# Kernel tuning notes

Measured on AMD Instinct MI355X. Metric: run time of the kernel, lower is better.

## Reference

```python
import jax, jax.numpy as jnp
import numpy as np

NUM_GROUPS = 32
EPS = 1e-5


def group_norm(x, w, b):
    # x: [B, C, H, W]
    B, C, H, W = x.shape
    g = x.reshape(B, NUM_GROUPS, C // NUM_GROUPS, H, W)
    mu = g.mean(axis=(2, 3, 4), keepdims=True)
    var = g.var(axis=(2, 3, 4), keepdims=True)
    g = (g - mu) * jax.lax.rsqrt(var + EPS)
    x = g.reshape(B, C, H, W)
    return x * w[None, :, None, None] + b[None, :, None, None]


def conv1x1(x, w, b):
    # 1x1 conv == channel matmul; x: [B, C, H, W], w: [O, C], b: [O]
    return jnp.einsum('bchw,oc->bohw', x, w) + b[None, :, None, None]


def setup_inputs() -> dict:
    key = jax.random.key(0)
    ks = jax.random.split(key, 11)
    C = 512
    B, H, W = 4, 64, 64
    s = 1.0 / np.sqrt(C)
    return {
        'x': jax.random.normal(ks[0], (B, C, H, W), jnp.float32),
        'gn_w': jax.random.uniform(ks[1], (C,), jnp.float32, 0.5, 1.5),
        'gn_b': jax.random.normal(ks[2], (C,), jnp.float32) * 0.1,
        'wq': jax.random.normal(ks[3], (C, C), jnp.float32) * s,
        'bq': jax.random.normal(ks[4], (C,), jnp.float32) * 0.01,
        'wk': jax.random.normal(ks[5], (C, C), jnp.float32) * s,
        'bk': jax.random.normal(ks[6], (C,), jnp.float32) * 0.01,
        'wv': jax.random.normal(ks[7], (C, C), jnp.float32) * s,
        'bv': jax.random.normal(ks[8], (C,), jnp.float32) * 0.01,
        'wo': jax.random.normal(ks[9], (C, C), jnp.float32) * s,
        'bo': jax.random.normal(ks[10], (C,), jnp.float32) * 0.01,
    }


def reference(x, gn_w, gn_b, wq, bq, wk, bk, wv, bv, wo, bo):
    B, C, H, W = x.shape
    h_ = group_norm(x, gn_w, gn_b)
    q = conv1x1(h_, wq, bq).reshape(B, C, H * W)   # [B, C, HW]
    k = conv1x1(h_, wk, bk).reshape(B, C, H * W)
    v = conv1x1(h_, wv, bv).reshape(B, C, H * W)
    # scores: q^T k, scaled by C^-0.5; softmax over keys
    scores = jnp.einsum('bci,bcj->bij', q, k) * (C ** -0.5)  # [B, HW, HW]
    attn = jax.nn.softmax(scores, axis=-1)
    # h_[b,c,i] = sum_j v[b,c,j] * attn[b,i,j]
    h_ = jnp.einsum('bcj,bij->bci', v, attn).reshape(B, C, H, W)
    return x + conv1x1(h_, wo, bo)
```

## Files before the change

### kernel.cpp

```cpp
#include <hip/hip_runtime.h>
#include <hip/hip_bf16.h>

typedef __attribute__((ext_vector_type(8))) __bf16 bf16x8;
typedef __attribute__((ext_vector_type(4))) float f32x4;

__device__ __forceinline__ unsigned short f2bf(float f) {
  union { float f; unsigned u; } v; v.f = f;
  unsigned r = v.u + 0x7fffu + ((v.u >> 16) & 1u);
  return (unsigned short)(r >> 16);
}

__device__ __forceinline__ void gload_lds16(const void* g, void* s) {
  __builtin_amdgcn_global_load_lds(
      (const __attribute__((address_space(1))) void*)g,
      (__attribute__((address_space(3))) void*)s, 16, 0, 0);
}

__global__ __launch_bounds__(256) void convert_w(
    const float* __restrict__ wq, const float* __restrict__ wk,
    const float* __restrict__ wv, const float* __restrict__ wo,
    unsigned short* __restrict__ dst) {
  const int m = blockIdx.x >> 10;
  const float* src = (m == 0) ? wq : (m == 1) ? wk : (m == 2) ? wv : wo;
  const int idx = ((blockIdx.x & 1023) << 8) | threadIdx.x;
  dst[m * 262144 + idx] = f2bf(src[idx]);
}

__global__ __launch_bounds__(256) void zero_k(float* __restrict__ p, int n) {
  const int i = blockIdx.x * 256 + threadIdx.x;
  if (i < n) p[i] = 0.f;
}

__global__ __launch_bounds__(256) void gn_stats(
    const float* __restrict__ x, float2* __restrict__ partials) {
  const int bg = blockIdx.x >> 2, part = blockIdx.x & 3;
  const float* xg = x + (size_t)bg * 65536 + part * 1024;
  const int t = threadIdx.x;
  float s = 0.f, ss = 0.f;
#pragma unroll
  for (int r = 0; r < 16; ++r) {
    const float4 v = *(const float4*)(xg + (size_t)r * 4096 + t * 4);
    s += v.x + v.y + v.z + v.w;
    ss += v.x * v.x + v.y * v.y + v.z * v.z + v.w * v.w;
  }
#pragma unroll
  for (int m = 32; m; m >>= 1) { s += __shfl_xor(s, m); ss += __shfl_xor(ss, m); }
  __shared__ float red[8];
  const int wave = t >> 6, lane = t & 63;
  if (lane == 0) { red[wave] = s; red[wave + 4] = ss; }
  __syncthreads();
  if (t == 0) {
    float2 p;
    p.x = red[0] + red[1] + red[2] + red[3];
    p.y = red[4] + red[5] + red[6] + red[7];
    partials[blockIdx.x] = p;
  }
}

__global__ __launch_bounds__(256) void gn_apply(
    const float* __restrict__ x, const float2* __restrict__ partials,
    const float* __restrict__ gw, const float* __restrict__ gb,
    unsigned short* __restrict__ h_t) {
  const int bg = blockIdx.x >> 3, cc = blockIdx.x & 7;
  const int b = bg >> 5, g = bg & 31;
  const int t = threadIdx.x;
  __shared__ float chs[32];
  __shared__ unsigned short tile[16][520];
  if (t < 16) {
    const float2 p0 = partials[bg * 4 + 0], p1 = partials[bg * 4 + 1];
    const float2 p2 = partials[bg * 4 + 2], p3 = partials[bg * 4 + 3];
    const float S = p0.x + p1.x + p2.x + p3.x;
    const float SS = p0.y + p1.y + p2.y + p3.y;
    const float mu = S * (1.f / 65536.f);
    const float rstd = rsqrtf(SS * (1.f / 65536.f) - mu * mu + 1e-5f);
    const float sc = gw[g * 16 + t] * rstd;
    chs[t] = sc;
    chs[16 + t] = gb[g * 16 + t] - mu * sc;
  }
  __syncthreads();
  const float* xg = x + (size_t)bg * 65536 + cc * 512;
#pragma unroll
  for (int rr = 0; rr < 8; ++rr) {
    const int r = rr * 2 + (t >> 7), i = (t & 127) * 4;
    const float4 v = *(const float4*)(xg + (size_t)r * 4096 + i);
    const float sc = chs[r], sh = chs[16 + r];
    ushort4 o;
    o.x = f2bf(v.x * sc + sh); o.y = f2bf(v.y * sc + sh);
    o.z = f2bf(v.z * sc + sh); o.w = f2bf(v.w * sc + sh);
    *(ushort4*)&tile[r][i] = o;
  }
  __syncthreads();
  unsigned short* outp = h_t + ((size_t)b * 4096 + cc * 512) * 512 + g * 16;
#pragma unroll
  for (int rep = 0; rep < 4; ++rep) {
    const int task = rep * 256 + t;
    const int nl = task >> 1, half = (task & 1) * 8;
    ushort4 o0, o1;
    o0.x = tile[half + 0][nl]; o0.y = tile[half + 1][nl];
    o0.z = tile[half + 2][nl]; o0.w = tile[half + 3][nl];
    o1.x = tile[half + 4][nl]; o1.y = tile[half + 5][nl];
    o1.z = tile[half + 6][nl]; o1.w = tile[half + 7][nl];
    *(ushort4*)(outp + (size_t)nl * 512 + half) = o0;
    *(ushort4*)(outp + (size_t)nl * 512 + half + 4) = o1;
  }
}

__global__ __launch_bounds__(256) void reduce4_k(
    const float* __restrict__ part, const float* __restrict__ l,
    unsigned short* __restrict__ dst) {
  const size_t i = ((size_t)blockIdx.x * 256 + threadIdx.x) * 4;
  f32x4 s0 = *(const f32x4*)(part + i);
  f32x4 s1 = *(const f32x4*)(part + 2097152 + i);
  f32x4 s2 = *(const f32x4*)(part + 4194304 + i);
  f32x4 s3 = *(const f32x4*)(part + 6291456 + i);
  f32x4 s = (s0 + s1) + (s2 + s3);
  const float inv = 1.f / l[i >> 9];
  ushort4 o;
  o.x = f2bf(s[0] * inv); o.y = f2bf(s[1] * inv);
  o.z = f2bf(s[2] * inv); o.w = f2bf(s[3] * inv);
  *(ushort4*)(dst + i) = o;
}

__global__ __launch_bounds__(512, 4) void gemm_s256(
    const unsigned short* __restrict__ A, const unsigned short* __restrict__ Bt,
    unsigned short* __restrict__ Out, float* __restrict__ lsum) {
  __shared__ __align__(16) char smem[73728];
  const int tid = threadIdx.x;
  const int wave = tid >> 6, lane = tid & 63;
  const int l15 = lane & 15, l4 = lane >> 4;
  const int wm = wave >> 1, wn = wave & 1;

  const int bz = blockIdx.z;
  A += (size_t)bz * 2097152;
  Bt += (size_t)bz * 2097152;
  Out += (size_t)bz * 16777216;
  lsum += (size_t)bz * 4096;

  const int id = blockIdx.y * 32 + blockIdx.x;
  const int xcd = id & 7, j = id >> 3;
  const int by = ((xcd >> 1) << 2) + (j >> 4);
  const int bx = ((xcd & 1) << 4) + (j & 15);
  const int row0 = by << 8, col0 = bx << 7;

  const int ar = tid >> 2;
  const int akc = (tid & 3) ^ ((tid >> 4) & 3);

  auto stage = [&](int kt, int bi) {
    const int kb = kt << 5;
    char* base = smem + bi * 24576;
    const unsigned short* gA = A + (size_t)(row0 + ar) * 512 + kb + akc * 8;
    const unsigned short* gB = Bt + (size_t)(col0 + ar) * 512 + kb + akc * 8;
    gload_lds16(gA, base + wave * 1024);
    gload_lds16(gA + (size_t)128 * 512, base + 8192 + wave * 1024);
    gload_lds16(gB, base + 16384 + wave * 1024);
  };

  f32x4 acc[4][4];
#pragma unroll
  for (int r = 0; r < 4; ++r)
#pragma unroll
    for (int c = 0; c < 4; ++c) acc[r][c] = (f32x4)0.f;

  const int xsw = (l4 ^ (l15 >> 2)) << 4;

  auto compute = [&](int bi) {
    const char* pa = smem + bi * 24576 + (wm * 64 + l15) * 64 + xsw;
    const char* pb = smem + bi * 24576 + 16384 + (wn * 64 + l15) * 64 + xsw;
    bf16x8 af[4], bfr[4];
#pragma unroll
    for (int r = 0; r < 4; ++r) af[r] = *(const bf16x8*)(pa + r * 1024);
#pragma unroll
    for (int c = 0; c < 4; ++c) bfr[c] = *(const bf16x8*)(pb + c * 1024);
#pragma unroll
    for (int r = 0; r < 4; ++r)
#pragma unroll
      for (int c = 0; c < 4; ++c)
        acc[r][c] = __builtin_amdgcn_mfma_f32_16x16x32_bf16(af[r], bfr[c], acc[r][c], 0, 0, 0);
  };

  stage(0, 0);
  stage(1, 1);
  int bi = 0;
  for (int kt = 0; kt < 15; ++kt) {
    asm volatile("s_waitcnt vmcnt(3)" ::: "memory");
    __builtin_amdgcn_s_barrier();
    __builtin_amdgcn_sched_barrier(0);
    if (kt + 2 < 16) stage(kt + 2, (kt + 2) % 3);
    compute(bi);
    bi = (bi == 2) ? 0 : bi + 1;
  }
  asm volatile("s_waitcnt vmcnt(0)" ::: "memory");
  __builtin_amdgcn_s_barrier();
  __builtin_amdgcn_sched_barrier(0);
  compute(bi);

  __syncthreads();
  unsigned short* tile = (unsigned short*)smem;
#pragma unroll
  for (int p = 0; p < 2; ++p) {
    if ((wm >> 1) == p) {
#pragma unroll
      for (int c = 0; c < 4; ++c) {
        const int coll = wn * 64 + c * 16 + l15;
#pragma unroll
        for (int r = 0; r < 4; ++r) {
          const int rowl = (wm & 1) * 64 + r * 16 + l4 * 4;
#pragma unroll
          for (int j = 0; j < 4; ++j)
            tile[(rowl + j) * 136 + coll] = f2bf(__expf(acc[r][c][j]));
        }
      }
    }
    __syncthreads();
#pragma unroll
    for (int it = 0; it < 4; ++it) {
      const int idx = it * 512 + tid;
      const int rw = idx >> 4, ch = (idx & 15) * 8;
      const uint4 vv = *(const uint4*)&tile[rw * 136 + ch];
      *(uint4*)(Out + (size_t)(row0 + p * 128 + rw) * 4096 + col0 + ch) = vv;
      const unsigned* uu = (const unsigned*)&vv;
      float s = 0.f;
#pragma unroll
      for (int q = 0; q < 4; ++q) {
        union { unsigned u; float f; } w;
        w.u = uu[q] << 16; s += w.f;
        w.u = uu[q] & 0xffff0000u; s += w.f;
      }
      s += __shfl_xor(s, 1); s += __shfl_xor(s, 2);
      s += __shfl_xor(s, 4); s += __shfl_xor(s, 8);
      if ((lane & 15) == 0) atomicAdd(&lsum[row0 + p * 128 + rw], s);
    }
    __syncthreads();
  }
}

__global__ __launch_bounds__(512, 2) void gemm_pv(
    const unsigned short* __restrict__ P, const unsigned short* __restrict__ Vt,
    unsigned short* __restrict__ Out, const float* __restrict__ lrow) {
  __shared__ __align__(16) char smem[147456];
  const int tid = threadIdx.x;
  const int wave = tid >> 6, lane = tid & 63;
  const int l15 = lane & 15, l4 = lane >> 4;
  const int wm = wave >> 1, wn = wave & 1;

  const int L = blockIdx.x + ((blockIdx.y + (blockIdx.z << 4)) << 2);
  const int xcd = L & 7, j = L >> 3;
  const int panel = xcd * 8 + (j >> 2);
  const int bx = j & 3, by = panel & 15, bz = panel >> 4;
  const int row0 = by << 8, col0 = bx << 7;
  P += (size_t)bz * 16777216;
  Vt += (size_t)bz * 2097152;
  Out += (size_t)bz * 2097152;
  lrow += bz * 4096;

  const int sr = tid >> 3;
  const int sc8 = (tid & 7) ^ (sr & 7);
  const unsigned short* gA = P + (size_t)(row0 + sr) * 4096 + sc8 * 8;
  const unsigned short* gB = Vt + (size_t)(col0 + sr) * 4096 + sc8 * 8;

  auto stA = [&](int kt, int bi, int p) {
    gload_lds16(gA + (size_t)(p << 6) * 4096 + (kt << 6),
                smem + bi * 49152 + p * 8192 + wave * 1024);
  };
  auto stB = [&](int kt, int bi, int p) {
    gload_lds16(gB + (size_t)(p << 6) * 4096 + (kt << 6),
                smem + bi * 49152 + 32768 + p * 8192 + wave * 1024);
  };

  f32x4 acc[4][4];
#pragma unroll
  for (int r = 0; r < 4; ++r)
#pragma unroll
    for (int c = 0; c < 4; ++c) acc[r][c] = (f32x4)0.f;

  const int sw0 = (l4 ^ (l15 & 7)) << 4;
  const int sw1 = ((4 + l4) ^ (l15 & 7)) << 4;
  const int arow = (wm * 64 + l15) << 7;
  const int brow = (wn * 64 + l15) << 7;

  bf16x8 bfr[4][2];

  stA(0, 0, 0); stA(0, 0, 1); stA(0, 0, 2); stA(0, 0, 3);
  stB(0, 0, 0); stB(0, 0, 1);
  stA(1, 1, 0); stA(1, 1, 1); stA(1, 1, 2); stA(1, 1, 3);
  stB(1, 1, 0); stB(1, 1, 1);
  asm volatile("s_waitcnt vmcnt(6)" ::: "memory");
  __builtin_amdgcn_s_barrier();
  __builtin_amdgcn_sched_barrier(0);

  int bi = 0;
#pragma unroll 1
  for (int kt = 0; kt < 64; ++kt) {
    const char* bufA = smem + bi * 49152;
    const char* bufB = bufA + 32768;
    const int pb = (bi + 2) % 3;
    const bool pre = (kt + 2 < 64);
    bf16x8 a0, a1;
    a0 = *(const bf16x8*)(bufA + arow + sw0);
    a1 = *(const bf16x8*)(bufA + arow + sw1);
#pragma unroll
    for (int c = 0; c < 4; ++c) {
      bfr[c][0] = *(const bf16x8*)(bufB + brow + c * 2048 + sw0);
      bfr[c][1] = *(const bf16x8*)(bufB + brow + c * 2048 + sw1);
    }
    if (pre) { stA(kt + 2, pb, 0); stA(kt + 2, pb, 1); }
    __builtin_amdgcn_s_barrier();
    asm volatile("s_waitcnt lgkmcnt(0)" ::: "memory");
    __builtin_amdgcn_sched_barrier(0);
    __builtin_amdgcn_s_setprio(1);
#pragma unroll
    for (int c = 0; c < 4; ++c) {
      acc[0][c] = __builtin_amdgcn_mfma_f32_16x16x32_bf16(a0, bfr[c][0], acc[0][c], 0, 0, 0);
      acc[0][c] = __builtin_amdgcn_mfma_f32_16x16x32_bf16(a1, bfr[c][1], acc[0][c], 0, 0, 0);
    }
    __builtin_amdgcn_s_setprio(0);
    __builtin_amdgcn_s_barrier();
    a0 = *(const bf16x8*)(bufA + arow + 2048 + sw0);
    a1 = *(const bf16x8*)(bufA + arow + 2048 + sw1);
    if (pre) { stA(kt + 2, pb, 2); stA(kt + 2, pb, 3); }
    __builtin_amdgcn_s_barrier();
    asm volatile("s_waitcnt lgkmcnt(0)" ::: "memory");
    __builtin_amdgcn_sched_barrier(0);
    __builtin_amdgcn_s_setprio(1);
#pragma unroll
    for (int c = 0; c < 4; ++c) {
      acc[1][c] = __builtin_amdgcn_mfma_f32_16x16x32_bf16(a0, bfr[c][0], acc[1][c], 0, 0, 0);
      acc[1][c] = __builtin_amdgcn_mfma_f32_16x16x32_bf16(a1, bfr[c][1], acc[1][c], 0, 0, 0);
    }
    __builtin_amdgcn_s_setprio(0);
    __builtin_amdgcn_s_barrier();
    a0 = *(const bf16x8*)(bufA + arow + 4096 + sw0);
    a1 = *(const bf16x8*)(bufA + arow + 4096 + sw1);
    if (pre) { stB(kt + 2, pb, 0); stB(kt + 2, pb, 1); }
    __builtin_amdgcn_s_barrier();
    asm volatile("s_waitcnt lgkmcnt(0)" ::: "memory");
    __builtin_amdgcn_sched_barrier(0);
    __builtin_amdgcn_s_setprio(1);
#pragma unroll
    for (int c = 0; c < 4; ++c) {
      acc[2][c] = __builtin_amdgcn_mfma_f32_16x16x32_bf16(a0, bfr[c][0], acc[2][c], 0, 0, 0);
      acc[2][c] = __builtin_amdgcn_mfma_f32_16x16x32_bf16(a1, bfr[c][1], acc[2][c], 0, 0, 0);
    }
    __builtin_amdgcn_s_setprio(0);
    __builtin_amdgcn_s_barrier();
    a0 = *(const bf16x8*)(bufA + arow + 6144 + sw0);
    a1 = *(const bf16x8*)(bufA + arow + 6144 + sw1);
    __builtin_amdgcn_s_barrier();
    asm volatile("s_waitcnt lgkmcnt(0)" ::: "memory");
    __builtin_amdgcn_sched_barrier(0);
    __builtin_amdgcn_s_setprio(1);
#pragma unroll
    for (int c = 0; c < 4; ++c) {
      acc[3][c] = __builtin_amdgcn_mfma_f32_16x16x32_bf16(a0, bfr[c][0], acc[3][c], 0, 0, 0);
      acc[3][c] = __builtin_amdgcn_mfma_f32_16x16x32_bf16(a1, bfr[c][1], acc[3][c], 0, 0, 0);
    }
    __builtin_amdgcn_s_setprio(0);
    if (pre) asm volatile("s_waitcnt vmcnt(6)" ::: "memory");
    else     asm volatile("s_waitcnt vmcnt(0)" ::: "memory");
    __builtin_amdgcn_s_barrier();
    __builtin_amdgcn_sched_barrier(0);
    bi = (bi == 2) ? 0 : bi + 1;
  }

  __syncthreads();
  unsigned short* tile = (unsigned short*)smem;
#pragma unroll
  for (int c = 0; c < 4; ++c) {
    const int coll = wn * 64 + c * 16 + l15;
#pragma unroll
    for (int r = 0; r < 4; ++r) {
      const int rowl = wm * 64 + r * 16 + l4 * 4;
#pragma unroll
      for (int j = 0; j < 4; ++j) {
        const float v = acc[r][c][j] * (1.0f / lrow[row0 + rowl + j]);
        tile[(rowl + j) * 136 + coll] = f2bf(v);
      }
    }
  }
  __syncthreads();
#pragma unroll
  for (int it = 0; it < 8; ++it) {
    const int idx = it * 512 + tid;
    const int rw = idx >> 4, ch = (idx & 15) * 8;
    const uint4 vv = *(const uint4*)&tile[rw * 136 + ch];
    *(uint4*)(Out + (size_t)(row0 + rw) * 512 + col0 + ch) = vv;
  }
}

template <bool OUT_BF16, int BIAS_MODE, bool RESID, bool TRANS_OUT, int SWZ,
          bool COAL>
__global__ __launch_bounds__(256) void gemm_bt(
    const unsigned short* __restrict__ A, long long sA, int lda,
    const unsigned short* __restrict__ Bt, long long sB, int ldb,
    void* __restrict__ OutV, long long sO, int ldo,
    const float* __restrict__ bias,
    const float* __restrict__ resid, long long sR,
    int K, float scale) {
  __shared__ __align__(16) char smem[49152];
  const int tid = threadIdx.x;
  const int wave = tid >> 6, lane = tid & 63;
  const int l15 = lane & 15, l4 = lane >> 4;
  const int wm = wave >> 1, wn = wave & 1;

  int bx = blockIdx.x, by = blockIdx.y, bz = blockIdx.z;
  if constexpr (SWZ == 1) {
    const int id = by * 32 + bx;
    const int xcd = id & 7, j = id >> 3;
    by = ((xcd >> 1) << 3) + (j >> 4);
    bx = ((xcd & 1) << 4) + (j & 15);
  } else if constexpr (SWZ == 2) {
    const int L = bx + ((by + (bz << 5)) << 2);
    const int xcd = L & 7, j = L >> 3;
    const int pair = xcd * 16 + (j >> 2);
    bx = j & 3;
    by = pair & 31;
    bz = pair >> 5;
  }
  const int row0 = by << 7, col0 = bx << 7;
  A += (size_t)bz * sA;
  Bt += (size_t)bz * sB;
  if (RESID) resid += (size_t)bz * sR;
  if constexpr (BIAS_MODE == 3) bias += (size_t)bz * sR;
  char* outB = (char*)OutV + (size_t)bz * sO * (OUT_BF16 ? 2 : 4);

  const int ar = tid >> 2;
  const int akc = (tid & 3) ^ ((tid >> 4) & 3);

  auto stage = [&](int kt, int bi) {
    const int kb = kt << 5;
    char* sAl = smem + bi * 16384 + wave * 1024;
    char* sBl = sAl + 8192;
    const unsigned short* gA = A + (size_t)(row0 + ar) * lda + kb + akc * 8;
    const unsigned short* gB = Bt + (size_t)(col0 + ar) * ldb + kb + akc * 8;
    gload_lds16(gA, sAl);
    gload_lds16(gB, sBl);
    gload_lds16(gA + (size_t)64 * lda, sAl + 4096);
    gload_lds16(gB + (size_t)64 * ldb, sBl + 4096);
  };

  f32x4 acc[4][4];
#pragma unroll
  for (int r = 0; r < 4; ++r)
#pragma unroll
    for (int c = 0; c < 4; ++c) acc[r][c] = (f32x4)0.f;

  const int nk = K >> 5;
  const int xsw = (l4 ^ (l15 >> 2)) << 4;

  auto compute = [&](int bi) {
    const char* pa = smem + bi * 16384 + (wm * 64 + l15) * 64 + xsw;
    const char* pb = smem + bi * 16384 + 8192 + (wn * 64 + l15) * 64 + xsw;
    bf16x8 af[4], bfr[4];
#pragma unroll
    for (int r = 0; r < 4; ++r) af[r] = *(const bf16x8*)(pa + r * 1024);
#pragma unroll
    for (int c = 0; c < 4; ++c) bfr[c] = *(const bf16x8*)(pb + c * 1024);
#pragma unroll
    for (int r = 0; r < 4; ++r)
#pragma unroll
      for (int c = 0; c < 4; ++c)
        acc[r][c] = __builtin_amdgcn_mfma_f32_16x16x32_bf16(af[r], bfr[c], acc[r][c], 0, 0, 0);
  };

  stage(0, 0);
  stage(1, 1);
  int bi = 0;
  for (int kt = 0; kt < nk - 1; ++kt) {
    asm volatile("s_waitcnt vmcnt(4)" ::: "memory");
    __builtin_amdgcn_s_barrier();
    __builtin_amdgcn_sched_barrier(0);
    if (kt + 2 < nk) stage(kt + 2, (kt + 2) % 3);
    compute(bi);
    bi = (bi == 2) ? 0 : bi + 1;
  }
  asm volatile("s_waitcnt vmcnt(0)" ::: "memory");
  __builtin_amdgcn_s_barrier();
  __builtin_amdgcn_sched_barrier(0);
  compute(bi);

  if constexpr (COAL && !TRANS_OUT) {
    __syncthreads();
    if constexpr (OUT_BF16) {
      unsigned short* tile = (unsigned short*)smem;
#pragma unroll
      for (int c = 0; c < 4; ++c) {
        const int coll = wn * 64 + c * 16 + l15;
        float badd = 0.f;
        if constexpr (BIAS_MODE == 1) badd = bias[col0 + coll];
#pragma unroll
        for (int r = 0; r < 4; ++r) {
          const int rowl = wm * 64 + r * 16 + l4 * 4;
#pragma unroll
          for (int j = 0; j < 4; ++j) {
            float v;
            if constexpr (BIAS_MODE == 3)
              v = acc[r][c][j] * (1.0f / bias[row0 + rowl + j]);
            else
              v = (acc[r][c][j] + badd) * scale;
            tile[(rowl + j) * 136 + coll] = f2bf(v);
          }
        }
      }
      __syncthreads();
      unsigned short* outp = (unsigned short*)outB;
#pragma unroll
      for (int it = 0; it < 8; ++it) {
        const int idx = it * 256 + tid;
        const int rw = idx >> 4, ch = (idx & 15) * 8;
        const uint4 vv = *(const uint4*)&tile[rw * 136 + ch];
        *(uint4*)(outp + (size_t)(row0 + rw) * ldo + col0 + ch) = vv;
      }
    } else {
      float* tile = (float*)smem;
#pragma unroll
      for (int p = 0; p < 2; ++p) {
        if (wm == p) {
#pragma unroll
          for (int c = 0; c < 4; ++c) {
            const int coll = wn * 64 + c * 16 + l15;
            float badd = 0.f;
            if constexpr (BIAS_MODE == 1) badd = bias[col0 + coll];
#pragma unroll
            for (int r = 0; r < 4; ++r) {
              const int rowl = r * 16 + l4 * 4;
#pragma unroll
              for (int j = 0; j < 4; ++j) {
                float v = acc[r][c][j] + badd;
                if constexpr (BIAS_MODE == 2) v += bias[row0 + p * 64 + rowl + j];
                tile[(rowl + j) * 132 + coll] = v * scale;
              }
            }
          }
        }
        __syncthreads();
        float* outp = (float*)outB;
#pragma unroll
        for (int it = 0; it < 8; ++it) {
          const int idx = it * 256 + tid;
          const int rw = idx >> 5, ch = (idx & 31) * 4;
          const int rowg = row0 + p * 64 + rw;
          f32x4 v = *(const f32x4*)&tile[rw * 132 + ch];
          if constexpr (RESID) {
            const float* rp = resid + (size_t)rowg * ldo + col0 + ch;
            v[0] += rp[0]; v[1] += rp[1]; v[2] += rp[2]; v[3] += rp[3];
          }
          *(f32x4*)(outp + (size_t)rowg * ldo + col0 + ch) = v;
        }
        __syncthreads();
      }
    }
  } else if constexpr (!TRANS_OUT) {
#pragma unroll
    for (int c = 0; c < 4; ++c) {
      const int colg = col0 + wn * 64 + c * 16 + l15;
      float badd = 0.f;
      if constexpr (BIAS_MODE == 1) badd = bias[colg];
#pragma unroll
      for (int r = 0; r < 4; ++r) {
        const int rowg = row0 + wm * 64 + r * 16 + l4 * 4;
#pragma unroll
        for (int j = 0; j < 4; ++j) {
          float v = acc[r][c][j] + badd;
          if constexpr (BIAS_MODE == 2) v += bias[rowg + j];
          v *= scale;
          if constexpr (RESID) v += resid[(size_t)(rowg + j) * ldo + colg];
          if constexpr (OUT_BF16)
            ((unsigned short*)outB)[(size_t)(rowg + j) * ldo + colg] = f2bf(v);
          else
            ((float*)outB)[(size_t)(rowg + j) * ldo + colg] = v;
        }
      }
    }
  } else {
    __syncthreads();
    unsigned short* tile = (unsigned short*)smem;
#pragma unroll
    for (int c = 0; c < 4; ++c) {
      const int coll = wn * 64 + c * 16 + l15;
      float badd = 0.f;
      if constexpr (BIAS_MODE == 1) badd = bias[col0 + coll];
#pragma unroll
      for (int r = 0; r < 4; ++r) {
        const int rowl = wm * 64 + r * 16 + l4 * 4;
#pragma unroll
        for (int j = 0; j < 4; ++j)
          tile[(rowl + j) * 132 + coll] = f2bf((acc[r][c][j] + badd) * scale);
      }
    }
    __syncthreads();
    unsigned short* outp = (unsigned short*)outB;
#pragma unroll 8
    for (int it = 0; it < 64; ++it) {
      const int idx = it * 256 + tid;
      const int cl = idx >> 7, il = idx & 127;
      outp[(size_t)(col0 + cl) * ldo + row0 + il] = tile[il * 132 + cl];
    }
  }
}

extern "C" void kernel_launch(void* const* d_in, const int* in_sizes, int n_in,
                              void* d_out, int out_size, void* d_ws, size_t ws_size,
                              hipStream_t stream) {
  const float* x   = (const float*)d_in[0];
  const float* gnw = (const float*)d_in[1];
  const float* gnb = (const float*)d_in[2];
  const float* wq  = (const float*)d_in[3];
  const float* bq  = (const float*)d_in[4];
  const float* wk  = (const float*)d_in[5];
  const float* bk  = (const float*)d_in[6];
  const float* wv  = (const float*)d_in[7];
  const float* bv  = (const float*)d_in[8];
  const float* wo  = (const float*)d_in[9];
  const float* bo  = (const float*)d_in[10];
  float* out = (float*)d_out;
  char* ws = (char*)d_ws;

  const size_t MB = 1u << 20;
  float2*         gnp  = (float2*)ws;
  float*          lrow = (float*)(ws + 64 * 1024);
  unsigned short* wbf  = (unsigned short*)(ws + 1 * MB);
  unsigned short* h_t  = (unsigned short*)(ws + 3 * MB);
  unsigned short* q_t  = (unsigned short*)(ws + 19 * MB);
  unsigned short* k_t  = (unsigned short*)(ws + 35 * MB);
  unsigned short* v_ct = (unsigned short*)(ws + 51 * MB);
  unsigned short* h2_t = (unsigned short*)(ws + 67 * MB);
  unsigned short* Pbuf = (unsigned short*)(ws + 83 * MB);
  float*          part = (float*)(ws + 115 * MB);

  const long long BS = 2097152;
  const long long PBS = 16777216;
  const float qscale = 0.044194173824159216f;
  const bool batched = ws_size >= 212 * MB;

  convert_w<<<dim3(4096), dim3(256), 0, stream>>>(wq, wk, wv, wo, wbf);
  gn_stats<<<dim3(512), dim3(256), 0, stream>>>(x, gnp);
  gn_apply<<<dim3(1024), dim3(256), 0, stream>>>(x, gnp, gnw, gnb, h_t);

  gemm_bt<true, 1, false, false, 0, true><<<dim3(4, 32, 4), 256, 0, stream>>>(
      h_t, BS, 512, wbf + 0, 0, 512, q_t, BS, 512, bq, nullptr, 0, 512, qscale);
  gemm_bt<true, 1, false, false, 0, true><<<dim3(4, 32, 4), 256, 0, stream>>>(
      h_t, BS, 512, wbf + 262144, 0, 512, k_t, BS, 512, bk, nullptr, 0, 512, 1.0f);
  gemm_bt<true, 1, false, true, 0, false><<<dim3(4, 32, 4), 256, 0, stream>>>(
      h_t, BS, 512, wbf + 524288, 0, 512, v_ct, BS, 4096, bv, nullptr, 0, 512, 1.0f);

  if (batched) {
    zero_k<<<dim3(64), dim3(256), 0, stream>>>(lrow, 16384);
    gemm_s256<<<dim3(32, 16, 4), dim3(512), 0, stream>>>(q_t, k_t, Pbuf, lrow);
    gemm_pv<<<dim3(4, 16, 4), dim3(512), 0, stream>>>(Pbuf, v_ct, h2_t, lrow);
  } else {
    for (int b = 0; b < 4; ++b) {
      zero_k<<<dim3(16), dim3(256), 0, stream>>>(lrow, 4096);
      gemm_s256<<<dim3(32, 16), dim3(512), 0, stream>>>(
          q_t + (size_t)b * BS, k_t + (size_t)b * BS, Pbuf, lrow);
      gemm_bt<false, 0, false, false, 0, true><<<dim3(4, 32, 4), 256, 0, stream>>>(
          Pbuf, 1024, 4096, v_ct + (size_t)b * BS, 1024, 4096,
          part, 2097152, 512, nullptr, nullptr, 0, 1024, 1.0f);
      reduce4_k<<<dim3(2048), dim3(256), 0, stream>>>(part, lrow, h2_t + (size_t)b * BS);
    }
  }

  gemm_bt<false, 2, true, false, 0, true><<<dim3(32, 4, 4), 256, 0, stream>>>(
      wbf + 786432, 0, 512, h2_t, BS, 512, out, BS, 4096, bo, x, BS, 512, 1.0f);
}
```

Before: 272.1 us.

## Add triple-buffered ping-pong score GEMM with XCD-aware tile mapping

Adds a new score-GEMM kernel, used on the batched path, that computes exp(QK^T) tiles with a three-stage LDS ring filled by direct global-to-LDS loads. Loads for later k-steps are interleaved between groups of MFMAs, with barriers and raised wave priority, so memory traffic overlaps compute. Blocks are remapped so that each XCD handles a contiguous region of the output, which should improve L2 reuse of Q and K. The cost is extra barriers per k-step and larger shared-memory use.

```diff
diff --git a/kernel.cpp b/kernel.cpp
--- a/kernel.cpp
+++ b/kernel.cpp
@@ -234,6 +234,170 @@
   }
 }
 
+__global__ __launch_bounds__(512, 2) void gemm_s_ps(
+    const unsigned short* __restrict__ A, const unsigned short* __restrict__ Bt,
+    unsigned short* __restrict__ Out, float* __restrict__ lsum) {
+  __shared__ __align__(16) char smem[147456];
+  const int tid = threadIdx.x;
+  const int wave = tid >> 6, lane = tid & 63;
+  const int l15 = lane & 15, l4 = lane >> 4;
+  const int wm = wave >> 1, wn = wave & 1;
+
+  const int bz = blockIdx.z;
+  A += (size_t)bz * 2097152;
+  Bt += (size_t)bz * 2097152;
+  Out += (size_t)bz * 16777216;
+  lsum += (size_t)bz * 4096;
+
+  const int id = blockIdx.y * 32 + blockIdx.x;
+  const int xcd = id & 7, j = id >> 3;
+  const int by = ((xcd >> 1) << 2) + (j >> 4);
+  const int bx = ((xcd & 1) << 4) + (j & 15);
+  const int row0 = by << 8, col0 = bx << 7;
+
+  const int sr = tid >> 3;
+  const int sc8 = (tid & 7) ^ (sr & 7);
+  const unsigned short* gA = A + (size_t)(row0 + sr) * 512 + sc8 * 8;
+  const unsigned short* gB = Bt + (size_t)(col0 + sr) * 512 + sc8 * 8;
+
+  auto stA = [&](int kt, int bi, int p) {
+    gload_lds16(gA + (size_t)(p << 6) * 512 + (kt << 6),
+                smem + bi * 49152 + p * 8192 + wave * 1024);
+  };
+  auto stB = [&](int kt, int bi, int p) {
+    gload_lds16(gB + (size_t)(p << 6) * 512 + (kt << 6),
+                smem + bi * 49152 + 32768 + p * 8192 + wave * 1024);
+  };
+
+  f32x4 acc[4][4];
+#pragma unroll
+  for (int r = 0; r < 4; ++r)
+#pragma unroll
+    for (int c = 0; c < 4; ++c) acc[r][c] = (f32x4)0.f;
+
+  const int sw0 = (l4 ^ (l15 & 7)) << 4;
+  const int sw1 = ((4 + l4) ^ (l15 & 7)) << 4;
+  const int arow = (wm * 64 + l15) << 7;
+  const int brow = (wn * 64 + l15) << 7;
+
+  bf16x8 bfr[4][2];
+
+  stA(0, 0, 0); stA(0, 0, 1); stA(0, 0, 2); stA(0, 0, 3);
+  stB(0, 0, 0); stB(0, 0, 1);
+  stA(1, 1, 0); stA(1, 1, 1); stA(1, 1, 2); stA(1, 1, 3);
+  stB(1, 1, 0); stB(1, 1, 1);
+  asm volatile("s_waitcnt vmcnt(6)" ::: "memory");
+  __builtin_amdgcn_s_barrier();
+  __builtin_amdgcn_sched_barrier(0);
+
+  int bi = 0;
+#pragma unroll 1
+  for (int kt = 0; kt < 8; ++kt) {
+    const char* bufA = smem + bi * 49152;
+    const char* bufB = bufA + 32768;
+    const int pb = (bi + 2) % 3;
+    const bool pre = (kt + 2 < 8);
+    bf16x8 a0, a1;
+    a0 = *(const bf16x8*)(bufA + arow + sw0);
+    a1 = *(const bf16x8*)(bufA + arow + sw1);
+#pragma unroll
+    for (int c = 0; c < 4; ++c) {
+      bfr[c][0] = *(const bf16x8*)(bufB + brow + c * 2048 + sw0);
+      bfr[c][1] = *(const bf16x8*)(bufB + brow + c * 2048 + sw1);
+    }
+    if (pre) { stA(kt + 2, pb, 0); stA(kt + 2, pb, 1); }
+    __builtin_amdgcn_s_barrier();
+    asm volatile("s_waitcnt lgkmcnt(0)" ::: "memory");
+    __builtin_amdgcn_sched_barrier(0);
+    __builtin_amdgcn_s_setprio(1);
+#pragma unroll
+    for (int c = 0; c < 4; ++c) {
+      acc[0][c] = __builtin_amdgcn_mfma_f32_16x16x32_bf16(a0, bfr[c][0], acc[0][c], 0, 0, 0);
+      acc[0][c] = __builtin_amdgcn_mfma_f32_16x16x32_bf16(a1, bfr[c][1], acc[0][c], 0, 0, 0);
+    }
+    __builtin_amdgcn_s_setprio(0);
+    __builtin_amdgcn_s_barrier();
+    a0 = *(const bf16x8*)(bufA + arow + 2048 + sw0);
+    a1 = *(const bf16x8*)(bufA + arow + 2048 + sw1);
+    if (pre) { stA(kt + 2, pb, 2); stA(kt + 2, pb, 3); }
+    __builtin_amdgcn_s_barrier();
+    asm volatile("s_waitcnt lgkmcnt(0)" ::: "memory");
+    __builtin_amdgcn_sched_barrier(0);
+    __builtin_amdgcn_s_setprio(1);
+#pragma unroll
+    for (int c = 0; c < 4; ++c) {
+      acc[1][c] = __builtin_amdgcn_mfma_f32_16x16x32_bf16(a0, bfr[c][0], acc[1][c], 0, 0, 0);
+      acc[1][c] = __builtin_amdgcn_mfma_f32_16x16x32_bf16(a1, bfr[c][1], acc[1][c], 0, 0, 0);
+    }
+    __builtin_amdgcn_s_setprio(0);
+    __builtin_amdgcn_s_barrier();
+    a0 = *(const bf16x8*)(bufA + arow + 4096 + sw0);
+    a1 = *(const bf16x8*)(bufA + arow + 4096 + sw1);
+    if (pre) { stB(kt + 2, pb, 0); stB(kt + 2, pb, 1); }
+    __builtin_amdgcn_s_barrier();
+    asm volatile("s_waitcnt lgkmcnt(0)" ::: "memory");
+    __builtin_amdgcn_sched_barrier(0);
+    __builtin_amdgcn_s_setprio(1);
+#pragma unroll
+    for (int c = 0; c < 4; ++c) {
+      acc[2][c] = __builtin_amdgcn_mfma_f32_16x16x32_bf16(a0, bfr[c][0], acc[2][c], 0, 0, 0);
+      acc[2][c] = __builtin_amdgcn_mfma_f32_16x16x32_bf16(a1, bfr[c][1], acc[2][c], 0, 0, 0);
+    }
+    __builtin_amdgcn_s_setprio(0);
+    __builtin_amdgcn_s_barrier();
+    a0 = *(const bf16x8*)(bufA + arow + 6144 + sw0);
+    a1 = *(const bf16x8*)(bufA + arow + 6144 + sw1);
+    __builtin_amdgcn_s_barrier();
+    asm volatile("s_waitcnt lgkmcnt(0)" ::: "memory");
+    __builtin_amdgcn_sched_barrier(0);
+    __builtin_amdgcn_s_setprio(1);
+#pragma unroll
+    for (int c = 0; c < 4; ++c) {
+      acc[3][c] = __builtin_amdgcn_mfma_f32_16x16x32_bf16(a0, bfr[c][0], acc[3][c], 0, 0, 0);
+      acc[3][c] = __builtin_amdgcn_mfma_f32_16x16x32_bf16(a1, bfr[c][1], acc[3][c], 0, 0, 0);
+    }
+    __builtin_amdgcn_s_setprio(0);
+    if (pre) asm volatile("s_waitcnt vmcnt(6)" ::: "memory");
+    else     asm volatile("s_waitcnt vmcnt(0)" ::: "memory");
+    __builtin_amdgcn_s_barrier();
+    __builtin_amdgcn_sched_barrier(0);
+    bi = (bi == 2) ? 0 : bi + 1;
+  }
+
+  __syncthreads();
+  unsigned short* tile = (unsigned short*)smem;
+#pragma unroll
+  for (int c = 0; c < 4; ++c) {
+    const int coll = wn * 64 + c * 16 + l15;
+#pragma unroll
+    for (int r = 0; r < 4; ++r) {
+      const int rowl = wm * 64 + r * 16 + l4 * 4;
+#pragma unroll
+      for (int j = 0; j < 4; ++j)
+        tile[(rowl + j) * 136 + coll] = f2bf(__expf(acc[r][c][j]));
+    }
+  }
+  __syncthreads();
+#pragma unroll
+  for (int it = 0; it < 8; ++it) {
+    const int idx = it * 512 + tid;
+    const int rw = idx >> 4, ch = (idx & 15) * 8;
+    const uint4 vv = *(const uint4*)&tile[rw * 136 + ch];
+    *(uint4*)(Out + (size_t)(row0 + rw) * 4096 + col0 + ch) = vv;
+    const unsigned* uu = (const unsigned*)&vv;
+    float s = 0.f;
+#pragma unroll
+    for (int q = 0; q < 4; ++q) {
+      union { unsigned u; float f; } w;
+      w.u = uu[q] << 16; s += w.f;
+      w.u = uu[q] & 0xffff0000u; s += w.f;
+    }
+    s += __shfl_xor(s, 1); s += __shfl_xor(s, 2);
+    s += __shfl_xor(s, 4); s += __shfl_xor(s, 8);
+    if ((lane & 15) == 0) atomicAdd(&lsum[row0 + rw], s);
+  }
+}
+
 __global__ __launch_bounds__(512, 2) void gemm_pv(
     const unsigned short* __restrict__ P, const unsigned short* __restrict__ Vt,
     unsigned short* __restrict__ Out, const float* __restrict__ lrow) {
@@ -645,12 +809,12 @@
 
   if (batched) {
     zero_k<<<dim3(64), dim3(256), 0, stream>>>(lrow, 16384);
-    gemm_s256<<<dim3(32, 16, 4), dim3(512), 0, stream>>>(q_t, k_t, Pbuf, lrow);
+    gemm_s_ps<<<dim3(32, 16, 4), dim3(512), 0, stream>>>(q_t, k_t, Pbuf, lrow);
     gemm_pv<<<dim3(4, 16, 4), dim3(512), 0, stream>>>(Pbuf, v_ct, h2_t, lrow);
   } else {
     for (int b = 0; b < 4; ++b) {
       zero_k<<<dim3(16), dim3(256), 0, stream>>>(lrow, 4096);
-      gemm_s256<<<dim3(32, 16), dim3(512), 0, stream>>>(
+      gemm_s256<<<dim3(32, 16, 1), dim3(512), 0, stream>>>(
           q_t + (size_t)b * BS, k_t + (size_t)b * BS, Pbuf, lrow);
       gemm_bt<false, 0, false, false, 0, true><<<dim3(4, 32, 4), 256, 0, stream>>>(
           Pbuf, 1024, 4096, v_ct + (size_t)b * BS, 1024, 4096,
```

New measurement: 295.9 us. 1.09x slower.
